# Kernel optimization log

Hardware: AMD Instinct MI355X
Metric: run time of the kernel (lower is better)

## Reference

```python
import jax, jax.numpy as jnp
import numpy as np

N, D = 8192, 512
LOGIT_SCALE = 2.659


def setup_inputs() -> dict:
    key = jax.random.key(0)
    k1, k2, k3 = jax.random.split(key, 3)
    text_features = jax.random.normal(k1, (N, D), dtype=jnp.float32)
    image_features = jax.random.normal(k2, (N, D), dtype=jnp.float32)
    labels = jax.random.randint(k3, (N,), 0, 100, dtype=jnp.int64)
    # sprinkle in some -1 (unlabeled) entries like the original supports
    labels = jnp.where(jax.random.uniform(jax.random.fold_in(key, 7), (N,)) < 0.1, -1, labels)
    return {"text_features": text_features, "image_features": image_features, "labels": labels}


def _l2_normalize(x):
    n = jnp.sqrt(jnp.sum(x * x, axis=-1, keepdims=True))
    return x / jnp.maximum(n, 1e-12)


def _soft_ce(s, t):
    # -(t * log softmax(s)).sum(-1) / t.sum(-1), averaged over rows
    loss = -jnp.sum(t * jax.nn.log_softmax(s, axis=-1), axis=-1)
    return jnp.mean(loss / jnp.sum(t, axis=-1))


def reference(text_features, image_features, labels):
    img = _l2_normalize(image_features)
    txt = _l2_normalize(text_features)
    logits_per_image = LOGIT_SCALE * (img @ txt.T)   # [N, N]
    logits_per_text = LOGIT_SCALE * (txt @ img.T)    # [N, N]

    # Vectorized equivalent of the per-row loop:
    # T[i,j] = 1 if i == j else (labels[i] == labels[j] and labels[i] != -1)
    eq = (labels[:, None] == labels[None, :]) & (labels[:, None] != -1)
    n = labels.shape[0]
    target = jnp.where(jnp.eye(n, dtype=bool), 1.0, eq.astype(jnp.float32))

    return (_soft_ce(logits_per_image, target) + _soft_ce(logits_per_text, target)) / 2
```

## Files before the change

### kernel.cpp

```cpp
#include <hip/hip_runtime.h>
#include <hip/hip_bf16.h>

#define N_ROWS 8192
#define DIM 512
#define SCALE 2.659f
#define MAXLOGIT 2.659f
#define LOG2E 1.4426950408889634f
#define BM 256
#define BN 256
#define NCLS 128
#define GEMM_BLKS 1024

typedef __attribute__((ext_vector_type(8))) short short8;
typedef __attribute__((ext_vector_type(4))) float f32x4;

#define ZERO_F4 36896

__device__ __forceinline__ unsigned short f2bf(float f) {
    unsigned int u = __float_as_uint(f);
    u += 0x7fffu + ((u >> 16) & 1u);
    return (unsigned short)(u >> 16);
}

__global__ __launch_bounds__(256) void norm_cast_kernel(
    const float* __restrict__ text, const float* __restrict__ image,
    const int* __restrict__ labels,
    unsigned short* __restrict__ imgn, unsigned short* __restrict__ txtn,
    float4* __restrict__ zbase, float* __restrict__ sd, float* __restrict__ out)
{
    int zi = blockIdx.x * 256 + threadIdx.x;
    if (zi < ZERO_F4) zbase[zi] = make_float4(0.f, 0.f, 0.f, 0.f);
    if (zi == 0) out[0] = 0.f;

    int row  = blockIdx.x * 4 + (threadIdx.x >> 6);
    int lane = threadIdx.x & 63;
    const float4* si = (const float4*)(image + (size_t)row * DIM) + lane * 2;
    const float4* st = (const float4*)(text  + (size_t)row * DIM) + lane * 2;
    float4 a = si[0], b = si[1], c = st[0], d = st[1];
    float ssa = a.x*a.x + a.y*a.y + a.z*a.z + a.w*a.w
              + b.x*b.x + b.y*b.y + b.z*b.z + b.w*b.w;
    float sst = c.x*c.x + c.y*c.y + c.z*c.z + c.w*c.w
              + d.x*d.x + d.y*d.y + d.z*d.z + d.w*d.w;
    float sab = a.x*c.x + a.y*c.y + a.z*c.z + a.w*c.w
              + b.x*d.x + b.y*d.y + b.z*d.z + b.w*d.w;
    #pragma unroll
    for (int m = 1; m < 64; m <<= 1) {
        ssa += __shfl_xor(ssa, m, 64);
        sst += __shfl_xor(sst, m, 64);
        sab += __shfl_xor(sab, m, 64);
    }
    float sca = 1.0f / fmaxf(sqrtf(ssa), 1e-12f);
    float sct = 1.0f / fmaxf(sqrtf(sst), 1e-12f);
    uint4 oi, ot;
    oi.x = (unsigned)f2bf(a.x*sca) | ((unsigned)f2bf(a.y*sca) << 16);
    oi.y = (unsigned)f2bf(a.z*sca) | ((unsigned)f2bf(a.w*sca) << 16);
    oi.z = (unsigned)f2bf(b.x*sca) | ((unsigned)f2bf(b.y*sca) << 16);
    oi.w = (unsigned)f2bf(b.z*sca) | ((unsigned)f2bf(b.w*sca) << 16);
    ot.x = (unsigned)f2bf(c.x*sct) | ((unsigned)f2bf(c.y*sct) << 16);
    ot.y = (unsigned)f2bf(c.z*sct) | ((unsigned)f2bf(c.w*sct) << 16);
    ot.z = (unsigned)f2bf(d.x*sct) | ((unsigned)f2bf(d.y*sct) << 16);
    ot.w = (unsigned)f2bf(d.z*sct) | ((unsigned)f2bf(d.w*sct) << 16);
    *((uint4*)(imgn + (size_t)row * DIM) + lane) = oi;
    *((uint4*)(txtn + (size_t)row * DIM) + lane) = ot;
    if (lane == 0)
        sd[row] = (labels[row] < 0) ? sab * sca * sct : 0.0f;
}

#define ASYNC16(gp, lp) \
  __builtin_amdgcn_global_load_lds((const __attribute__((address_space(1))) void*)(gp), \
                                   (__attribute__((address_space(3))) void*)(lp), 16, 0, 0)

#define SFENCE __builtin_amdgcn_sched_barrier(0)

#define STAGE(b, k0)                                                          \
  {                                                                           \
    const unsigned short* Ap = A + (size_t)(rowBase + w*16 + srow) * DIM      \
                                 + (k0) + spart;                              \
    const unsigned short* Bp = B + (size_t)(colBase + w*16 + srow) * DIM      \
                                 + (k0) + spart;                              \
    ASYNC16(Ap,             &Ald[b][(w*16) * 32]);                            \
    ASYNC16(Ap + 128 * DIM, &Ald[b][(128 + w*16) * 32]);                      \
    ASYNC16(Bp,             &Bld[b][(w*16) * 32]);                            \
    ASYNC16(Bp + 128 * DIM, &Bld[b][(128 + w*16) * 32]);                      \
  }

__global__ __launch_bounds__(512, 2) void gemm_fused_kernel(
    const unsigned short* __restrict__ imgn, const unsigned short* __restrict__ txtn,
    const int* __restrict__ labels,
    float* __restrict__ rs, float* __restrict__ cs,
    float* __restrict__ c_txt, float* __restrict__ c_img, int* __restrict__ cnt)
{
    __shared__ unsigned short Ald[4][BM * 32];
    __shared__ unsigned short Bld[4][BN * 32];
    __shared__ float red[4][BM];
    __shared__ float colb[2][BN];
    __shared__ int   list[1024];
    __shared__ int   lcount;

    int tid  = threadIdx.x;

    if (blockIdx.x >= GEMM_BLKS) {
        int blk = blockIdx.x - GEMM_BLKS;
        int cls = blk & (NCLS - 1);
        int mat = blk >> 7;
        const unsigned* src = (const unsigned*)(mat ? imgn : txtn);
        float* dst = mat ? c_img : c_txt;
        if (tid == 0) lcount = 0;
        __syncthreads();
        #pragma unroll
        for (int base = 0; base < N_ROWS; base += 512) {
            int lb = labels[base + tid];
            if (lb == cls) { int s = atomicAdd(&lcount, 1); list[s & 1023] = base + tid; }
        }
        __syncthreads();
        int m = lcount;
        if (mat == 0 && tid == 0) cnt[cls] = m;
        int half = tid >> 8;
        int col  = tid & 255;
        float a0 = 0.f, a1 = 0.f;
        int r = half;
        for (; r + 6 < m; r += 8) {
            unsigned u0 = src[(size_t)list[r]   * (DIM/2) + col];
            unsigned u1 = src[(size_t)list[r+2] * (DIM/2) + col];
            unsigned u2 = src[(size_t)list[r+4] * (DIM/2) + col];
            unsigned u3 = src[(size_t)list[r+6] * (DIM/2) + col];
            a0 += __uint_as_float((u0 & 0xffffu) << 16) + __uint_as_float((u1 & 0xffffu) << 16)
                + __uint_as_float((u2 & 0xffffu) << 16) + __uint_as_float((u3 & 0xffffu) << 16);
            a1 += __uint_as_float(u0 & 0xffff0000u) + __uint_as_float(u1 & 0xffff0000u)
                + __uint_as_float(u2 & 0xffff0000u) + __uint_as_float(u3 & 0xffff0000u);
        }
        for (; r < m; r += 2) {
            unsigned u = src[(size_t)list[r] * (DIM/2) + col];
            a0 += __uint_as_float((u & 0xffffu) << 16);
            a1 += __uint_as_float(u & 0xffff0000u);
        }
        if (a0 != 0.f || a1 != 0.f) {
            unsafeAtomicAdd(&dst[(size_t)cls * DIM + col*2],     a0);
            unsafeAtomicAdd(&dst[(size_t)cls * DIM + col*2 + 1], a1);
        }
        return;
    }

    int bid    = blockIdx.x;
    int rowblk = bid & 31;
    int colblk = bid >> 5;
    const unsigned short* A = imgn;
    const unsigned short* B = txtn;
    int rowBase = rowblk * BM;
    int colBase = colblk * BN;

    int lane = tid & 63;
    int w    = tid >> 6;
    int wr   = w >> 2, wc = w & 3;
    int q    = lane >> 4;
    int lm   = lane & 15;

    int srow  = lane >> 2;
    int spart = (lane & 3) * 8;

    const float C1 = SCALE * LOG2E;
    const float C2 = -MAXLOGIT * LOG2E;

    f32x4 acc[8][4];
    #pragma unroll
    for (int mi = 0; mi < 8; ++mi)
      #pragma unroll
      for (int ni = 0; ni < 4; ++ni)
        acc[mi][ni] = (f32x4){0.f, 0.f, 0.f, 0.f};

    STAGE(0, 0);
    STAGE(1, 32);
    SFENCE;
    asm volatile("s_waitcnt vmcnt(4)" ::: "memory");
    SFENCE;
    __builtin_amdgcn_s_barrier();
    SFENCE;

    #pragma unroll
    for (int g = 0; g < DIM / 32; ++g) {
        const int bcur = g & 3;
        const int bpf  = (g + 2) & 3;
        if (g + 2 < DIM / 32) {
            STAGE(bpf, (g + 2) * 32);
        }

        short8 af[8], bf[4];
        #pragma unroll
        for (int mi = 0; mi < 8; ++mi)
            af[mi] = *(const short8*)(&Ald[bcur][(wr*128 + mi*16 + lm)*32 + q*8]);
        #pragma unroll
        for (int ni = 0; ni < 4; ++ni)
            bf[ni] = *(const short8*)(&Bld[bcur][(wc*64 + ni*16 + lm)*32 + q*8]);
        #pragma unroll
        for (int mi = 0; mi < 8; ++mi)
          #pragma unroll
          for (int ni = 0; ni < 4; ++ni)
            acc[mi][ni] = __builtin_amdgcn_mfma_f32_16x16x32_bf16(
                              af[mi], bf[ni], acc[mi][ni], 0, 0, 0);

        SFENCE;
        if (g + 2 < DIM / 32) asm volatile("s_waitcnt vmcnt(4)" ::: "memory");
        else                  asm volatile("s_waitcnt vmcnt(0)" ::: "memory");
        SFENCE;
        __builtin_amdgcn_s_barrier();
        SFENCE;
    }

    float rsum[32];
    #pragma unroll
    for (int i = 0; i < 32; ++i) rsum[i] = 0.f;
    #pragma unroll
    for (int ni = 0; ni < 4; ++ni) {
        float csum = 0.f;
        #pragma unroll
        for (int mi = 0; mi < 8; ++mi) {
          #pragma unroll
          for (int r = 0; r < 4; ++r) {
            float e = __builtin_amdgcn_exp2f(fmaf(acc[mi][ni][r], C1, C2));
            rsum[mi*4 + r] += e;
            csum += e;
          }
        }
        csum += __shfl_xor(csum, 16, 64);
        csum += __shfl_xor(csum, 32, 64);
        if (q == 0)
            colb[wr][wc*64 + ni*16 + lm] = csum;
    }
    #pragma unroll
    for (int idx = 0; idx < 32; ++idx) {
        float s = rsum[idx];
        #pragma unroll
        for (int m = 1; m < 16; m <<= 1) s += __shfl_xor(s, m, 64);
        if (lm == 0)
            red[wc][wr*128 + (idx>>2)*16 + q*4 + (idx&3)] = s;
    }
    __syncthreads();
    if (tid < BM) {
        unsafeAtomicAdd(&rs[rowBase + tid],
                        red[0][tid] + red[1][tid] + red[2][tid] + red[3][tid]);
        unsafeAtomicAdd(&cs[colBase + tid], colb[0][tid] + colb[1][tid]);
    }
}

__global__ __launch_bounds__(256) void loss_tail_kernel(
    const float* __restrict__ rs, const float* __restrict__ cs,
    const float* __restrict__ sd, const float* __restrict__ c_txt,
    const float* __restrict__ c_img, const int* __restrict__ cnt,
    float* __restrict__ out)
{
    __shared__ float wsum[4];
    int tid = threadIdx.x, lane = tid & 63, w = tid >> 6;
    int gidx = blockIdx.x * 256 + tid;
    float local;
    if (gidx < N_ROWS)
        local = (MAXLOGIT + logf(rs[gidx])) - 2.0f * SCALE * sd[gidx];
    else
        local = MAXLOGIT + logf(cs[gidx - N_ROWS]);

    int cls = blockIdx.x * 2 + (tid >> 7);
    int e0  = (tid & 127) * 4;
    int n   = cnt[cls];
    if (n > 0) {
        float4 x = *(const float4*)(c_txt + (size_t)cls * DIM + e0);
        float4 y = *(const float4*)(c_img + (size_t)cls * DIM + e0);
        float dotp = x.x*y.x + x.y*y.y + x.z*y.z + x.w*y.w;
        local -= 2.0f * SCALE * dotp / (float)n;
    }

    #pragma unroll
    for (int m = 1; m < 64; m <<= 1) local += __shfl_xor(local, m, 64);
    if (lane == 0) wsum[w] = local;
    __syncthreads();
    if (tid == 0)
        unsafeAtomicAdd(out, (wsum[0] + wsum[1] + wsum[2] + wsum[3])
                             * (1.0f / (2 * N_ROWS)));
}

extern "C" void kernel_launch(void* const* d_in, const int* in_sizes, int n_in,
                              void* d_out, int out_size, void* d_ws, size_t ws_size,
                              hipStream_t stream)
{
    const float* text   = (const float*)d_in[0];
    const float* image  = (const float*)d_in[1];
    const int*   labels = (const int*)d_in[2];

    unsigned short* imgn = (unsigned short*)d_ws;
    unsigned short* txtn = imgn + (size_t)N_ROWS * DIM;
    char* p = (char*)d_ws + 2 * (size_t)N_ROWS * DIM * sizeof(unsigned short);
    float* rs    = (float*)p;
    float* cs    = rs + N_ROWS;
    float* c_txt = cs + N_ROWS;
    float* c_img = c_txt + (size_t)NCLS * DIM;
    int*   cnt   = (int*)(c_img + (size_t)NCLS * DIM);
    float* sd    = (float*)(cnt + NCLS);
    float* out = (float*)d_out;

    hipLaunchKernelGGL(norm_cast_kernel, dim3(N_ROWS / 4), dim3(256), 0, stream,
                       text, image, labels, imgn, txtn, (float4*)rs, sd, out);
    hipLaunchKernelGGL(gemm_fused_kernel, dim3(GEMM_BLKS + 2 * NCLS), dim3(512), 0, stream,
                       imgn, txtn, labels, rs, cs, c_txt, c_img, cnt);
    hipLaunchKernelGGL(loss_tail_kernel, dim3(64), dim3(256), 0, stream,
                       rs, cs, sd, c_txt, c_img, cnt, out);
}
```

Baseline: 168.2 us.

## Restructure GEMM main loop to K=64 double-buffered tiles with XOR swizzle and split staging

The GEMM main loop moves from four 32-wide K buffers to two 64-wide K buffers, each split into 128-row halves. Global-to-LDS loads are interleaved at finer granularity between the MFMA groups, and an XOR swizzle on the LDS layout is meant to avoid bank conflicts on fragment reads. MFMA sections are bracketed with s_setprio so compute waves get priority. The aim is fewer loop iterations and barriers per K element, and better overlap of loads with compute, at the cost of more barriers inside each iteration and trickier vmcnt accounting.

New measurement: 174.4 us. 1.04x slower.

```diff
diff --git a/kernel.cpp b/kernel.cpp
--- a/kernel.cpp
+++ b/kernel.cpp
@@ -71,17 +71,41 @@
                                    (__attribute__((address_space(3))) void*)(lp), 16, 0, 0)
 
 #define SFENCE __builtin_amdgcn_sched_barrier(0)
-
-#define STAGE(b, k0)                                                          \
+#define BARRIER { SFENCE; __builtin_amdgcn_s_barrier(); SFENCE; }
+
+#define STG_A(db_, h_, kofs_)                                                 \
   {                                                                           \
-    const unsigned short* Ap = A + (size_t)(rowBase + w*16 + srow) * DIM      \
-                                 + (k0) + spart;                              \
-    const unsigned short* Bp = B + (size_t)(colBase + w*16 + srow) * DIM      \
-                                 + (k0) + spart;                              \
-    ASYNC16(Ap,             &Ald[b][(w*16) * 32]);                            \
-    ASYNC16(Ap + 128 * DIM, &Ald[b][(128 + w*16) * 32]);                      \
-    ASYNC16(Bp,             &Bld[b][(w*16) * 32]);                            \
-    ASYNC16(Bp + 128 * DIM, &Bld[b][(128 + w*16) * 32]);                      \
+    const unsigned short* _p = A + (size_t)(rowBase + (h_)*128 + w*16 + srow8) * DIM \
+                                 + (kofs_) + swz8;                            \
+    ASYNC16(_p,           &Ald[db_][h_][w*1024]);                             \
+    ASYNC16(_p + 8*DIM,   &Ald[db_][h_][w*1024 + 512]);                       \
+  }
+#define STG_B(db_, h_, kofs_)                                                 \
+  {                                                                           \
+    const unsigned short* _p = B + (size_t)(colBase + (h_)*128 + w*16 + srow8) * DIM \
+                                 + (kofs_) + swz8;                            \
+    ASYNC16(_p,           &Bld[db_][h_][w*1024]);                             \
+    ASYNC16(_p + 8*DIM,   &Bld[db_][h_][w*1024 + 512]);                       \
+  }
+
+#define LDA8(db_, kk_)                                                        \
+  _Pragma("unroll")                                                           \
+  for (int mi = 0; mi < 8; ++mi)                                              \
+      af[mi] = *(const short8*)(&Ald[db_][wr][(mi*16 + lm)*64 +               \
+                                (((kk_<<2)|q) ^ (lm & 7))*8]);
+#define LDB(db_, kk_, ni_)                                                    \
+  (*(const short8*)(&Bld[db_][hb][((wc&1)*64 + (ni_)*16 + lm)*64 +            \
+                                  (((kk_<<2)|q) ^ (lm & 7))*8]))
+#define MM2(n0_, n1_, b0_, b1_)                                               \
+  {                                                                           \
+    __builtin_amdgcn_s_setprio(1);                                            \
+    _Pragma("unroll")                                                         \
+    for (int mi = 0; mi < 8; ++mi)                                            \
+        acc[mi][n0_] = __builtin_amdgcn_mfma_f32_16x16x32_bf16(af[mi], b0_, acc[mi][n0_], 0, 0, 0); \
+    _Pragma("unroll")                                                         \
+    for (int mi = 0; mi < 8; ++mi)                                            \
+        acc[mi][n1_] = __builtin_amdgcn_mfma_f32_16x16x32_bf16(af[mi], b1_, acc[mi][n1_], 0, 0, 0); \
+    __builtin_amdgcn_s_setprio(0);                                            \
   }
 
 __global__ __launch_bounds__(512, 2) void gemm_fused_kernel(
@@ -90,14 +114,14 @@
     float* __restrict__ rs, float* __restrict__ cs,
     float* __restrict__ c_txt, float* __restrict__ c_img, int* __restrict__ cnt)
 {
-    __shared__ unsigned short Ald[4][BM * 32];
-    __shared__ unsigned short Bld[4][BN * 32];
+    __shared__ unsigned short Ald[2][2][128 * 64];
+    __shared__ unsigned short Bld[2][2][128 * 64];
     __shared__ float red[4][BM];
     __shared__ float colb[2][BN];
     __shared__ int   list[1024];
     __shared__ int   lcount;
 
-    int tid  = threadIdx.x;
+    int tid = threadIdx.x;
 
     if (blockIdx.x >= GEMM_BLKS) {
         int blk = blockIdx.x - GEMM_BLKS;
@@ -151,12 +175,14 @@
 
     int lane = tid & 63;
     int w    = tid >> 6;
-    int wr   = w >> 2, wc = w & 3;
+    int wr   = w >> 2;
+    int wc   = w & 3;
+    int hb   = wc >> 1;
     int q    = lane >> 4;
     int lm   = lane & 15;
 
-    int srow  = lane >> 2;
-    int spart = (lane & 3) * 8;
+    int srow8 = lane >> 3;
+    int swz8  = (((lane & 7) ^ ((lane >> 3) & 7)) * 8);
 
     const float C1 = SCALE * LOG2E;
     const float C2 = -MAXLOGIT * LOG2E;
@@ -168,42 +194,54 @@
       for (int ni = 0; ni < 4; ++ni)
         acc[mi][ni] = (f32x4){0.f, 0.f, 0.f, 0.f};
 
-    STAGE(0, 0);
-    STAGE(1, 32);
+    STG_A(0, 0, 0);
+    STG_A(0, 1, 0);
+    STG_B(0, 0, 0);
+    STG_B(0, 1, 0);
+    STG_A(1, 0, 64);
     SFENCE;
-    asm volatile("s_waitcnt vmcnt(4)" ::: "memory");
-    SFENCE;
-    __builtin_amdgcn_s_barrier();
-    SFENCE;
-
-    #pragma unroll
-    for (int g = 0; g < DIM / 32; ++g) {
-        const int bcur = g & 3;
-        const int bpf  = (g + 2) & 3;
-        if (g + 2 < DIM / 32) {
-            STAGE(bpf, (g + 2) * 32);
-        }
-
-        short8 af[8], bf[4];
-        #pragma unroll
-        for (int mi = 0; mi < 8; ++mi)
-            af[mi] = *(const short8*)(&Ald[bcur][(wr*128 + mi*16 + lm)*32 + q*8]);
-        #pragma unroll
-        for (int ni = 0; ni < 4; ++ni)
-            bf[ni] = *(const short8*)(&Bld[bcur][(wc*64 + ni*16 + lm)*32 + q*8]);
-        #pragma unroll
-        for (int mi = 0; mi < 8; ++mi)
-          #pragma unroll
-          for (int ni = 0; ni < 4; ++ni)
-            acc[mi][ni] = __builtin_amdgcn_mfma_f32_16x16x32_bf16(
-                              af[mi], bf[ni], acc[mi][ni], 0, 0, 0);
-
+    asm volatile("s_waitcnt vmcnt(0)" ::: "memory");
+    BARRIER;
+
+    short8 af[8];
+
+    #pragma unroll
+    for (int t = 0; t < DIM / 64; ++t) {
+        const int db = t & 1;
+        const int dn = (t + 1) & 1;
+        const int k0 = t * 64;
+
+        if (t + 1 < 8) { STG_A(dn, 1, k0 + 64); STG_B(dn, 0, k0 + 64); }
+        LDA8(db, 0);
+        {
+            short8 b0 = LDB(db, 0, 0), b1 = LDB(db, 0, 1);
+            MM2(0, 1, b0, b1);
+        }
+        BARRIER;
+
+        if (t + 1 < 8) STG_B(dn, 1, k0 + 64);
+        {
+            short8 b2 = LDB(db, 0, 2), b3 = LDB(db, 0, 3);
+            MM2(2, 3, b2, b3);
+        }
+        BARRIER;
+
+        LDA8(db, 1);
+        {
+            short8 b0 = LDB(db, 1, 0), b1 = LDB(db, 1, 1);
+            MM2(0, 1, b0, b1);
+        }
+        BARRIER;
+
+        if (t + 2 < 8) STG_A(db, 0, k0 + 128);
+        {
+            short8 b2 = LDB(db, 1, 2), b3 = LDB(db, 1, 3);
+            MM2(2, 3, b2, b3);
+        }
         SFENCE;
-        if (g + 2 < DIM / 32) asm volatile("s_waitcnt vmcnt(4)" ::: "memory");
-        else                  asm volatile("s_waitcnt vmcnt(0)" ::: "memory");
-        SFENCE;
-        __builtin_amdgcn_s_barrier();
-        SFENCE;
+        if (t < 6) asm volatile("s_waitcnt vmcnt(2)" ::: "memory");
+        else       asm volatile("s_waitcnt vmcnt(0)" ::: "memory");
+        BARRIER;
     }
 
     float rsum[32];
```

## Shrink GEMM tile to 256x128 with 4 waves, swizzle LDS, split class-sum blocks

Applied to the files above, without the earlier changes.

Switches the fused GEMM from 512-thread 256x256 tiles to 256-thread 256x128 tiles, doubling the number of GEMM blocks. It drops to triple-buffered LDS staging and adds an XOR swizzle on the K-chunk offsets to reduce LDS bank conflicts on the fragment reads. The class-centroid blocks are split into 8 label slices of 1024 each, with atomics accumulating the counts, and slices with no matches return early. Each wave still computes a 128x64 sub-tile, so per-block reuse of the A operand falls and atomic traffic on the column sums grows.

Result: slower. 172.9 us (+2.8%).

```diff
diff --git a/kernel.cpp b/kernel.cpp
--- a/kernel.cpp
+++ b/kernel.cpp
@@ -7,9 +7,9 @@
 #define MAXLOGIT 2.659f
 #define LOG2E 1.4426950408889634f
 #define BM 256
-#define BN 256
+#define BN 128
 #define NCLS 128
-#define GEMM_BLKS 1024
+#define GEMM_BLKS 2048
 
 typedef __attribute__((ext_vector_type(8))) short short8;
 typedef __attribute__((ext_vector_type(4))) float f32x4;
@@ -75,69 +75,71 @@
 #define STAGE(b, k0)                                                          \
   {                                                                           \
     const unsigned short* Ap = A + (size_t)(rowBase + w*16 + srow) * DIM      \
-                                 + (k0) + spart;                              \
+                                 + (k0) + spsw;                               \
     const unsigned short* Bp = B + (size_t)(colBase + w*16 + srow) * DIM      \
-                                 + (k0) + spart;                              \
+                                 + (k0) + spsw;                               \
     ASYNC16(Ap,             &Ald[b][(w*16) * 32]);                            \
+    ASYNC16(Ap +  64 * DIM, &Ald[b][( 64 + w*16) * 32]);                      \
     ASYNC16(Ap + 128 * DIM, &Ald[b][(128 + w*16) * 32]);                      \
+    ASYNC16(Ap + 192 * DIM, &Ald[b][(192 + w*16) * 32]);                      \
     ASYNC16(Bp,             &Bld[b][(w*16) * 32]);                            \
-    ASYNC16(Bp + 128 * DIM, &Bld[b][(128 + w*16) * 32]);                      \
+    ASYNC16(Bp +  64 * DIM, &Bld[b][( 64 + w*16) * 32]);                      \
   }
 
-__global__ __launch_bounds__(512, 2) void gemm_fused_kernel(
+__global__ __launch_bounds__(256, 2) void gemm_fused_kernel(
     const unsigned short* __restrict__ imgn, const unsigned short* __restrict__ txtn,
     const int* __restrict__ labels,
     float* __restrict__ rs, float* __restrict__ cs,
     float* __restrict__ c_txt, float* __restrict__ c_img, int* __restrict__ cnt)
 {
-    __shared__ unsigned short Ald[4][BM * 32];
-    __shared__ unsigned short Bld[4][BN * 32];
-    __shared__ float red[4][BM];
+    __shared__ unsigned short Ald[3][BM * 32];
+    __shared__ unsigned short Bld[3][BN * 32];
+    __shared__ float red[2][BM];
     __shared__ float colb[2][BN];
     __shared__ int   list[1024];
     __shared__ int   lcount;
 
-    int tid  = threadIdx.x;
+    int tid = threadIdx.x;
 
     if (blockIdx.x >= GEMM_BLKS) {
         int blk = blockIdx.x - GEMM_BLKS;
         int cls = blk & (NCLS - 1);
-        int mat = blk >> 7;
+        int mat = (blk >> 7) & 1;
+        int slc = blk >> 8;
         const unsigned* src = (const unsigned*)(mat ? imgn : txtn);
         float* dst = mat ? c_img : c_txt;
         if (tid == 0) lcount = 0;
         __syncthreads();
-        #pragma unroll
-        for (int base = 0; base < N_ROWS; base += 512) {
-            int lb = labels[base + tid];
-            if (lb == cls) { int s = atomicAdd(&lcount, 1); list[s & 1023] = base + tid; }
+        int base0 = slc * 1024;
+        #pragma unroll
+        for (int it = 0; it < 4; ++it) {
+            int i  = base0 + it * 256 + tid;
+            int lb = labels[i];
+            if (lb == cls) { int s = atomicAdd(&lcount, 1); list[s & 1023] = i; }
         }
         __syncthreads();
         int m = lcount;
-        if (mat == 0 && tid == 0) cnt[cls] = m;
-        int half = tid >> 8;
-        int col  = tid & 255;
+        if (m == 0) return;
+        if (mat == 0 && tid == 0) atomicAdd(&cnt[cls], m);
         float a0 = 0.f, a1 = 0.f;
-        int r = half;
-        for (; r + 6 < m; r += 8) {
-            unsigned u0 = src[(size_t)list[r]   * (DIM/2) + col];
-            unsigned u1 = src[(size_t)list[r+2] * (DIM/2) + col];
-            unsigned u2 = src[(size_t)list[r+4] * (DIM/2) + col];
-            unsigned u3 = src[(size_t)list[r+6] * (DIM/2) + col];
+        int r = 0;
+        for (; r + 4 <= m; r += 4) {
+            unsigned u0 = src[(size_t)list[r]   * (DIM/2) + tid];
+            unsigned u1 = src[(size_t)list[r+1] * (DIM/2) + tid];
+            unsigned u2 = src[(size_t)list[r+2] * (DIM/2) + tid];
+            unsigned u3 = src[(size_t)list[r+3] * (DIM/2) + tid];
             a0 += __uint_as_float((u0 & 0xffffu) << 16) + __uint_as_float((u1 & 0xffffu) << 16)
                 + __uint_as_float((u2 & 0xffffu) << 16) + __uint_as_float((u3 & 0xffffu) << 16);
             a1 += __uint_as_float(u0 & 0xffff0000u) + __uint_as_float(u1 & 0xffff0000u)
                 + __uint_as_float(u2 & 0xffff0000u) + __uint_as_float(u3 & 0xffff0000u);
         }
-        for (; r < m; r += 2) {
-            unsigned u = src[(size_t)list[r] * (DIM/2) + col];
+        for (; r < m; ++r) {
+            unsigned u = src[(size_t)list[r] * (DIM/2) + tid];
             a0 += __uint_as_float((u & 0xffffu) << 16);
             a1 += __uint_as_float(u & 0xffff0000u);
         }
-        if (a0 != 0.f || a1 != 0.f) {
-            unsafeAtomicAdd(&dst[(size_t)cls * DIM + col*2],     a0);
-            unsafeAtomicAdd(&dst[(size_t)cls * DIM + col*2 + 1], a1);
-        }
+        unsafeAtomicAdd(&dst[(size_t)cls * DIM + tid*2],     a0);
+        unsafeAtomicAdd(&dst[(size_t)cls * DIM + tid*2 + 1], a1);
         return;
     }
 
@@ -151,12 +153,14 @@
 
     int lane = tid & 63;
     int w    = tid >> 6;
-    int wr   = w >> 2, wc = w & 3;
+    int wr   = w >> 1;
+    int wc   = w & 1;
     int q    = lane >> 4;
     int lm   = lane & 15;
-
-    int srow  = lane >> 2;
-    int spart = (lane & 3) * 8;
+    int qa   = q ^ ((lm >> 1) & 3);
+
+    int srow = lane >> 2;
+    int spsw = (((lane & 3) ^ ((lane >> 3) & 3)) * 8);
 
     const float C1 = SCALE * LOG2E;
     const float C2 = -MAXLOGIT * LOG2E;
@@ -171,15 +175,15 @@
     STAGE(0, 0);
     STAGE(1, 32);
     SFENCE;
-    asm volatile("s_waitcnt vmcnt(4)" ::: "memory");
+    asm volatile("s_waitcnt vmcnt(6)" ::: "memory");
     SFENCE;
     __builtin_amdgcn_s_barrier();
     SFENCE;
 
     #pragma unroll
     for (int g = 0; g < DIM / 32; ++g) {
-        const int bcur = g & 3;
-        const int bpf  = (g + 2) & 3;
+        const int bcur = g % 3;
+        const int bpf  = (g + 2) % 3;
         if (g + 2 < DIM / 32) {
             STAGE(bpf, (g + 2) * 32);
         }
@@ -187,10 +191,10 @@
         short8 af[8], bf[4];
         #pragma unroll
         for (int mi = 0; mi < 8; ++mi)
-            af[mi] = *(const short8*)(&Ald[bcur][(wr*128 + mi*16 + lm)*32 + q*8]);
+            af[mi] = *(const short8*)(&Ald[bcur][(wr*128 + mi*16 + lm)*32 + qa*8]);
         #pragma unroll
         for (int ni = 0; ni < 4; ++ni)
-            bf[ni] = *(const short8*)(&Bld[bcur][(wc*64 + ni*16 + lm)*32 + q*8]);
+            bf[ni] = *(const short8*)(&Bld[bcur][(wc*64 + ni*16 + lm)*32 + qa*8]);
         #pragma unroll
         for (int mi = 0; mi < 8; ++mi)
           #pragma unroll
@@ -199,7 +203,7 @@
                               af[mi], bf[ni], acc[mi][ni], 0, 0, 0);
 
         SFENCE;
-        if (g + 2 < DIM / 32) asm volatile("s_waitcnt vmcnt(4)" ::: "memory");
+        if (g + 2 < DIM / 32) asm volatile("s_waitcnt vmcnt(6)" ::: "memory");
         else                  asm volatile("s_waitcnt vmcnt(0)" ::: "memory");
         SFENCE;
         __builtin_amdgcn_s_barrier();
@@ -235,11 +239,9 @@
             red[wc][wr*128 + (idx>>2)*16 + q*4 + (idx&3)] = s;
     }
     __syncthreads();
-    if (tid < BM) {
-        unsafeAtomicAdd(&rs[rowBase + tid],
-                        red[0][tid] + red[1][tid] + red[2][tid] + red[3][tid]);
+    unsafeAtomicAdd(&rs[rowBase + tid], red[0][tid] + red[1][tid]);
+    if (tid < BN)
         unsafeAtomicAdd(&cs[colBase + tid], colb[0][tid] + colb[1][tid]);
-    }
 }
 
 __global__ __launch_bounds__(256) void loss_tail_kernel(
@@ -297,7 +299,7 @@
 
     hipLaunchKernelGGL(norm_cast_kernel, dim3(N_ROWS / 4), dim3(256), 0, stream,
                        text, image, labels, imgn, txtn, (float4*)rs, sd, out);
-    hipLaunchKernelGGL(gemm_fused_kernel, dim3(GEMM_BLKS + 2 * NCLS), dim3(512), 0, stream,
+    hipLaunchKernelGGL(gemm_fused_kernel, dim3(GEMM_BLKS + 2048), dim3(256), 0, stream,
                        imgn, txtn, labels, rs, cs, c_txt, c_img, cnt);
     hipLaunchKernelGGL(loss_tail_kernel, dim3(64), dim3(256), 0, stream,
                        rs, cs, sd, c_txt, c_img, cnt, out);
```
